# Performance work log

Measured on AMD Instinct MI355X. Metric: run time of the kernel, lower is better.

The kernel has to match this reference:

```python
import jax, jax.numpy as jnp
import numpy as np

S, B, H, T = 1024, 32, 1024, 512


def setup_inputs() -> dict:
    key = jax.random.key(0)
    ks = jax.random.split(key, 7)
    scale = 1.0 / np.sqrt(H)
    return {
        "hidden": jax.random.normal(ks[0], (S, B, H), dtype=jnp.float32),
        "x": jax.random.normal(ks[1], (B, T, H), dtype=jnp.float32),
        "problem_q": jax.random.normal(ks[2], (B, H), dtype=jnp.float32),
        "K_w": jax.random.normal(ks[3], (H, H), dtype=jnp.float32) * scale,
        "K_b": jax.random.normal(ks[4], (H,), dtype=jnp.float32) * scale,
        "V_w": jax.random.normal(ks[5], (H, H), dtype=jnp.float32) * scale,
        "V_b": jax.random.normal(ks[6], (H,), dtype=jnp.float32) * scale,
    }


def reference(hidden, x, problem_q, K_w, K_b, V_w, V_b):
    # hidden: [S, B, H] -> hidden2: [B, S, H]
    hidden2 = jnp.transpose(hidden, (1, 0, 2))
    # Linear projections (torch Linear: y = x @ W.T + b)
    k = jnp.einsum("bsh,kh->bsk", hidden2, K_w) + K_b  # [B, S, H]
    v = jnp.einsum("bsh,kh->bsk", hidden2, V_w) + V_b  # [B, S, H]
    # scores[b,t,s] = x[b,t] . k[b,s]  (QK^T per batch)
    scores = jnp.einsum("bth,bsh->bts", x, k)
    attn = jax.nn.softmax(scores, axis=-1)  # softmax over encoder positions S
    out = jax.nn.sigmoid(jnp.einsum("bts,bsh->bth", attn, v))  # [B, T, H]
    return out
```

## Files before the change

kernel.cpp:

```cpp
#include <hip/hip_runtime.h>

typedef unsigned short u16;
typedef __attribute__((ext_vector_type(8))) short short8;
typedef __attribute__((ext_vector_type(8))) _Float16 half8;
typedef __attribute__((ext_vector_type(4))) float f32x4;
typedef __attribute__((ext_vector_type(4))) u16 u16x4;
typedef __attribute__((ext_vector_type(4))) unsigned int u32x4;

#define DEVINL static __device__ __forceinline__

DEVINL u16 f2bf(float f) {
  unsigned u = __builtin_bit_cast(unsigned, f);
  u += 0x7fffu + ((u >> 16) & 1u);
  return (u16)(u >> 16);
}
DEVINL float bf2f(u16 h) {
  return __builtin_bit_cast(float, ((unsigned)h) << 16);
}
DEVINL u16 f2h(float f) { return __builtin_bit_cast(u16, (_Float16)f); }
DEVINL float h2f(u16 h) { return (float)__builtin_bit_cast(_Float16, h); }

DEVINL void gload16(const void* g, void* l) {
  __builtin_amdgcn_global_load_lds(
      (const __attribute__((address_space(1))) void*)g,
      (__attribute__((address_space(3))) void*)l, 16, 0, 0);
}

#define BAR() asm volatile("s_barrier" ::: "memory")
#define WAIT_VMN(n) asm volatile("s_waitcnt vmcnt(" #n ")" ::: "memory")
#define WAIT_VM_LGKM0() asm volatile("s_waitcnt vmcnt(0) lgkmcnt(0)" ::: "memory")


__global__ __launch_bounds__(512) void cvt_hidden2_k(const float* __restrict__ hid,
                                                     u16* __restrict__ hf,
                                                     u16* __restrict__ hT) {
  __shared__ u16 tl[64][136];
  const int s0 = blockIdx.x * 64;
  const int h0 = blockIdx.y * 128;
  const int b = blockIdx.z;
  const int t = threadIdx.x;
  const int r = t >> 5;
  const int c4 = (t & 31) * 4;
#pragma unroll
  for (int it = 0; it < 4; ++it) {
    const int s = it * 16 + r;
    const f32x4 v = *(const f32x4*)(hid + ((size_t)(s0 + s) * 32 + b) * 1024 + h0 + c4);
    u16x4 of;
    const int cs = c4 ^ (it << 2);
#pragma unroll
    for (int j = 0; j < 4; ++j) {
      of[j] = f2h(v[j]);
      tl[s][cs + j] = f2bf(v[j]);
    }
    *(u16x4*)(hf + ((size_t)b * 1024 + s0 + s) * 1024 + h0 + c4) = of;
  }
  __syncthreads();
  const int h = t >> 2;
  const int sq = (t & 3) * 16;
  u16 tmp[16] __attribute__((aligned(16)));
#pragma unroll
  for (int i = 0; i < 16; ++i)
    tmp[i] = tl[sq + i][h ^ ((((sq + i) >> 4) & 3) << 2)];
  u16* dst = hT + ((size_t)b * 1024 + h0 + h) * 1024 + s0 + sq;
  *(u32x4*)(dst) = *(const u32x4*)&tmp[0];
  *(u32x4*)(dst + 8) = *(const u32x4*)&tmp[8];
}

__global__ __launch_bounds__(256) void cvt_f32_bf16_k(const float* __restrict__ in,
                                                      u16* __restrict__ out, long n4) {
  long i = (long)blockIdx.x * 256 + threadIdx.x;
  const long stride = (long)gridDim.x * 256;
  for (; i < n4; i += stride) {
    const f32x4 v = ((const f32x4*)in)[i];
    u16x4 o;
#pragma unroll
    for (int j = 0; j < 4; ++j) o[j] = f2bf(v[j]);
    ((u16x4*)out)[i] = o;
  }
}

__global__ __launch_bounds__(256) void cvt_w_t_h_k(const float* __restrict__ in,
                                                   u16* __restrict__ out) {
  __shared__ float tile[64][65];
  const int bh = blockIdx.x * 64;
  const int bj = blockIdx.y * 64;
  const int t = threadIdx.x;
  const int r = t >> 4;
  const int c4 = (t & 15) * 4;
#pragma unroll
  for (int it = 0; it < 4; ++it) {
    const int row = it * 16 + r;
    const f32x4 v = *(const f32x4*)(in + (size_t)(bj + row) * 1024 + bh + c4);
#pragma unroll
    for (int j = 0; j < 4; ++j) tile[c4 + j][row] = v[j];
  }
  __syncthreads();
#pragma unroll
  for (int it = 0; it < 4; ++it) {
    const int hrow = it * 16 + r;
    u16x4 of;
#pragma unroll
    for (int j = 0; j < 4; ++j) of[j] = f2h(tile[hrow][c4 + j]);
    *(u16x4*)(out + (size_t)(bh + hrow) * 1024 + bj + c4) = of;
  }
}

__global__ __launch_bounds__(512) void gemm_qp_k(
    const float* __restrict__ X, const u16* __restrict__ Bm,
    u16* __restrict__ Chi, u16* __restrict__ Clo) {
  __shared__ u16 lA[2][256 * 64];
  __shared__ u16 lB[2][256 * 32];
  const int bid = blockIdx.x;
  const int swz = (bid & 7) * 32 + (bid >> 3);
  const int m0 = (swz >> 2) * 256;
  const int n0 = (swz & 3) * 256;
  const int tid = threadIdx.x;
  const int lane = tid & 63, wid = tid >> 6;
  const int wr = wid >> 2, wc = wid & 3;
  const int fr = lane & 15, fk = lane >> 4;

  f32x4 acc[8][4] = {};

#define STAGEAF(pb, kt)                                                        \
  {                                                                            \
    _Pragma("unroll") for (int j = 0; j < 2; ++j) {                            \
      const int ps = j * 512 + tid;                                            \
      const int r = ps >> 2, q = ps & 3;                                       \
      const float* src = X + (size_t)(m0 + r) * 1024 + (kt) * 32 + q * 8;      \
      const f32x4 v0 = *(const f32x4*)src;                                     \
      const f32x4 v1 = *(const f32x4*)(src + 4);                               \
      short8 hs, ls;                                                           \
      _Pragma("unroll") for (int e = 0; e < 4; ++e) {                          \
        const u16 a0 = f2h(v0[e]);                                             \
        const u16 a1 = f2h(v1[e]);                                             \
        hs[e] = (short)a0;                                                     \
        hs[e + 4] = (short)a1;                                                 \
        ls[e] = (short)f2h(v0[e] - h2f(a0));                                   \
        ls[e + 4] = (short)f2h(v1[e] - h2f(a1));                               \
      }                                                                        \
      const int c = q ^ (r & 7);                                               \
      *(short8*)&lA[pb][r * 64 + c * 8] = hs;                                  \
      *(short8*)&lA[pb][r * 64 + (c ^ 4) * 8] = ls;                            \
    }                                                                          \
  }
#define STAGEB(pb, kt)                                                         \
  {                                                                            \
    _Pragma("unroll") for (int j = 0; j < 2; ++j) {                            \
      const int slot = j * 512 + tid;                                          \
      const int r = slot >> 2;                                                 \
      const int g = (slot & 3) ^ ((r >> 1) & 3);                               \
      gload16(Bm + (size_t)(n0 + r) * 1024 + (kt) * 32 + g * 8,                \
              &lB[pb][(j * 512 + wid * 64) * 8]);                              \
    }                                                                          \
  }

  STAGEAF(0, 0);
  STAGEB(0, 0);

  for (int t = 0; t < 32; ++t) {
    const int p = t & 1;
    WAIT_VM_LGKM0();
    BAR();
    half8 bf[4];
#pragma unroll
    for (int nf = 0; nf < 4; ++nf) {
      const int rn = wc * 64 + nf * 16 + fr;
      const int cn = fk ^ ((rn >> 1) & 3);
      bf[nf] = *(const half8*)&lB[p][rn * 32 + cn * 8];
    }
    if (t < 31) {
      STAGEB(p ^ 1, t + 1);
      STAGEAF(p ^ 1, t + 1);
    }
#pragma unroll
    for (int ph = 0; ph < 4; ++ph) {
      half8 ah[2], al[2];
#pragma unroll
      for (int i = 0; i < 2; ++i) {
        const int r = wr * 128 + (ph * 2 + i) * 16 + fr;
        const int ch = fk ^ (r & 7);
        ah[i] = *(const half8*)&lA[p][r * 64 + ch * 8];
        al[i] = *(const half8*)&lA[p][r * 64 + (ch ^ 4) * 8];
      }
      __builtin_amdgcn_s_setprio(1);
#pragma unroll
      for (int i = 0; i < 2; ++i)
#pragma unroll
        for (int nf = 0; nf < 4; ++nf) {
          acc[ph * 2 + i][nf] =
              __builtin_amdgcn_mfma_f32_16x16x32_f16(ah[i], bf[nf], acc[ph * 2 + i][nf], 0, 0, 0);
          acc[ph * 2 + i][nf] =
              __builtin_amdgcn_mfma_f32_16x16x32_f16(al[i], bf[nf], acc[ph * 2 + i][nf], 0, 0, 0);
        }
      __builtin_amdgcn_s_setprio(0);
    }
  }
#undef STAGEAF
#undef STAGEB

  const int cb = n0 + wc * 64 + fr;
  const int rb = m0 + wr * 128 + fk * 4;
#pragma unroll
  for (int mf = 0; mf < 8; ++mf)
#pragma unroll
    for (int nf = 0; nf < 4; ++nf) {
      const int col = cb + nf * 16;
#pragma unroll
      for (int j = 0; j < 4; ++j) {
        const int row = rb + mf * 16 + j;
        const float kv = acc[mf][nf][j];
        const u16 hi = f2h(kv);
        Chi[(size_t)row * 1024 + col] = hi;
        Clo[(size_t)row * 1024 + col] = f2h(kv - h2f(hi));
      }
    }
}

__global__ __launch_bounds__(512) void gemm_sc_k(
    const u16* __restrict__ Qh_, const u16* __restrict__ Ql_,
    const u16* __restrict__ Hf_, float* __restrict__ S) {
  __shared__ u16 lA[3][256 * 64];
  __shared__ u16 lB[3][256 * 32];
  const int bid = blockIdx.x;
  const int swz = (bid & 7) * 32 + (bid >> 3);
  const int z = swz >> 3;
  const int m0 = ((swz >> 2) & 1) * 256;
  const int n0 = (swz & 3) * 256;
  const u16* Ah = Qh_ + (size_t)z * 512 * 1024;
  const u16* Al = Ql_ + (size_t)z * 512 * 1024;
  const u16* Bm = Hf_ + (size_t)z * 1024 * 1024;
  float* Cf = S + (size_t)z * 512 * 1024;
  const int tid = threadIdx.x;
  const int lane = tid & 63, wid = tid >> 6;
  const int wr = wid >> 2, wc = wid & 3;
  const int fr = lane & 15, fk = lane >> 4;

  f32x4 acc[8][4] = {};

#define STAGEA(pb, kt)                                                         \
  {                                                                            \
    _Pragma("unroll") for (int j = 0; j < 4; ++j) {                            \
      const int slot = j * 512 + tid;                                          \
      const int r = slot >> 3;                                                 \
      const int g = (slot & 7) ^ (r & 7);                                      \
      const u16* src = (g < 4) ? Ah : Al;                                      \
      gload16(src + (size_t)(m0 + r) * 1024 + (kt) * 32 + (g & 3) * 8,         \
              &lA[pb][(j * 512 + wid * 64) * 8]);                              \
    }                                                                          \
  }
#define STAGEB(pb, kt)                                                         \
  {                                                                            \
    _Pragma("unroll") for (int j = 0; j < 2; ++j) {                            \
      const int slot = j * 512 + tid;                                          \
      const int r = slot >> 2;                                                 \
      const int g = (slot & 3) ^ ((r >> 1) & 3);                               \
      gload16(Bm + (size_t)(n0 + r) * 1024 + (kt) * 32 + g * 8,                \
              &lB[pb][(j * 512 + wid * 64) * 8]);                              \
    }                                                                          \
  }

  STAGEA(0, 0);
  STAGEB(0, 0);
  STAGEA(1, 1);
  STAGEB(1, 1);

  int cur = 0;
  for (int t = 0; t < 32; ++t) {
    if (t < 31) {
      WAIT_VMN(6);
    } else {
      WAIT_VMN(0);
    }
    BAR();
    int pre = cur + 2;
    if (pre >= 3) pre -= 3;
    half8 bf[4];
#pragma unroll
    for (int nf = 0; nf < 4; ++nf) {
      const int rn = wc * 64 + nf * 16 + fr;
      const int cn = fk ^ ((rn >> 1) & 3);
      bf[nf] = *(const half8*)&lB[cur][rn * 32 + cn * 8];
    }
    if (t < 30) {
      STAGEA(pre, t + 2);
      STAGEB(pre, t + 2);
    }
#pragma unroll
    for (int ph = 0; ph < 4; ++ph) {
      half8 ah[2], al[2];
#pragma unroll
      for (int i = 0; i < 2; ++i) {
        const int r = wr * 128 + (ph * 2 + i) * 16 + fr;
        const int ch = fk ^ (r & 7);
        ah[i] = *(const half8*)&lA[cur][r * 64 + ch * 8];
        al[i] = *(const half8*)&lA[cur][r * 64 + (ch ^ 4) * 8];
      }
      __builtin_amdgcn_s_setprio(1);
#pragma unroll
      for (int i = 0; i < 2; ++i)
#pragma unroll
        for (int nf = 0; nf < 4; ++nf) {
          acc[ph * 2 + i][nf] =
              __builtin_amdgcn_mfma_f32_16x16x32_f16(ah[i], bf[nf], acc[ph * 2 + i][nf], 0, 0, 0);
          acc[ph * 2 + i][nf] =
              __builtin_amdgcn_mfma_f32_16x16x32_f16(al[i], bf[nf], acc[ph * 2 + i][nf], 0, 0, 0);
        }
      __builtin_amdgcn_s_setprio(0);
    }
    ++cur;
    if (cur == 3) cur = 0;
  }
#undef STAGEA
#undef STAGEB

  const int cb = n0 + wc * 64 + fr;
  const int rb = m0 + wr * 128 + fk * 4;
#pragma unroll
  for (int mf = 0; mf < 8; ++mf)
#pragma unroll
    for (int nf = 0; nf < 4; ++nf) {
      const int col = cb + nf * 16;
#pragma unroll
      for (int j = 0; j < 4; ++j) {
        const int row = rb + mf * 16 + j;
        Cf[(size_t)row * 1024 + col] = acc[mf][nf][j];
      }
    }
}

template <int CM>
__global__ __launch_bounds__(512) void gemm1_8ph_k(
    const u16* __restrict__ A_, const u16* __restrict__ Bt_,
    const float* __restrict__ bias, void* __restrict__ Cout) {
  __shared__ u16 lds[2][2][256 * 64];
  const int bid = blockIdx.x;
  const int swz = (bid & 7) * 32 + (bid >> 3);
  int m0, n0;
  const u16 *A, *Bt;
  float* Cf = nullptr;
  u16* Cb = nullptr;
  if (CM == 0) {
    const int z = swz >> 3;
    m0 = ((swz >> 2) & 1) * 256;
    n0 = (swz & 3) * 256;
    A = A_ + (size_t)z * 512 * 1024;
    Bt = Bt_ + (size_t)z * 1024 * 1024;
    Cb = (u16*)Cout + (size_t)z * 512 * 1024;
  } else {
    m0 = (swz >> 2) * 256;
    n0 = (swz & 3) * 256;
    A = A_; Bt = Bt_;
    Cf = (float*)Cout;
  }
  const int tid = threadIdx.x;
  const int lane = tid & 63, wid = tid >> 6;
  const int wr = wid >> 2, wc = wid & 3;
  const int fr = lane & 15, fk = lane >> 4;

  f32x4 acc[8][4] = {};

#define STAGE1(pb, q, gp, rb, kt)                                              \
  {                                                                            \
    _Pragma("unroll") for (int j = 0; j < 4; ++j) {                            \
      const int slot = j * 512 + tid;                                          \
      const int r = slot >> 3;                                                 \
      const int g = (slot & 7) ^ (r & 7);                                      \
      gload16((gp) + (size_t)((rb) + r) * 1024 + (kt) * 64 + g * 8,            \
              &lds[pb][q][(j * 512 + wid * 64) * 8]);                          \
    }                                                                          \
  }

  STAGE1(0, 0, A, m0, 0);
  STAGE1(0, 1, Bt, n0, 0);

  for (int t = 0; t < 16; ++t) {
    const int p = t & 1;
    WAIT_VMN(0);
    BAR();
    short8 bfr[4][2];
#pragma unroll
    for (int nf = 0; nf < 4; ++nf) {
      const int rn = wc * 64 + nf * 16 + fr;
#pragma unroll
      for (int ks = 0; ks < 2; ++ks) {
        const int g = (ks * 4 + fk) ^ (rn & 7);
        bfr[nf][ks] = *(const short8*)&lds[p][1][rn * 64 + g * 8];
      }
    }
    if (t < 15) {
      STAGE1(p ^ 1, 0, A, m0, t + 1);
      STAGE1(p ^ 1, 1, Bt, n0, t + 1);
    }
#pragma unroll
    for (int ph = 0; ph < 4; ++ph) {
      short8 a[2][2];
#pragma unroll
      for (int i = 0; i < 2; ++i) {
        const int r = wr * 128 + (ph * 2 + i) * 16 + fr;
#pragma unroll
        for (int ks = 0; ks < 2; ++ks) {
          const int g = (ks * 4 + fk) ^ (r & 7);
          a[i][ks] = *(const short8*)&lds[p][0][r * 64 + g * 8];
        }
      }
      __builtin_amdgcn_s_setprio(1);
#pragma unroll
      for (int i = 0; i < 2; ++i)
#pragma unroll
        for (int nf = 0; nf < 4; ++nf) {
          acc[ph * 2 + i][nf] = __builtin_amdgcn_mfma_f32_16x16x32_bf16(
              a[i][0], bfr[nf][0], acc[ph * 2 + i][nf], 0, 0, 0);
          acc[ph * 2 + i][nf] = __builtin_amdgcn_mfma_f32_16x16x32_bf16(
              a[i][1], bfr[nf][1], acc[ph * 2 + i][nf], 0, 0, 0);
        }
      __builtin_amdgcn_s_setprio(0);
    }
  }
#undef STAGE1

  const int cb = n0 + wc * 64 + fr;
  const int rb = m0 + wr * 128 + fk * 4;
  if (CM == 0) {
#pragma unroll
    for (int mf = 0; mf < 8; ++mf)
#pragma unroll
      for (int nf = 0; nf < 4; ++nf) {
        const int col = cb + nf * 16;
#pragma unroll
        for (int j = 0; j < 4; ++j) {
          const int row = rb + mf * 16 + j;
          Cb[(size_t)row * 1024 + col] = f2bf(acc[mf][nf][j]);
        }
      }
  } else {
#pragma unroll
    for (int mf = 0; mf < 8; ++mf)
#pragma unroll
      for (int nf = 0; nf < 4; ++nf) {
        const int col = cb + nf * 16;
        const float bv = bias[col];
#pragma unroll
        for (int j = 0; j < 4; ++j) {
          const int row = rb + mf * 16 + j;
          const float xv = acc[mf][nf][j] + bv;
          Cf[(size_t)row * 1024 + col] = 1.0f / (1.0f + __expf(-xv));
        }
      }
  }
}

__global__ __launch_bounds__(256) void softmax_k(const float* __restrict__ S,
                                                 u16* __restrict__ Attn) {
  const float* rp = S + (size_t)blockIdx.x * 1024;
  const int tid = threadIdx.x;
  const int lane = tid & 63, wid = tid >> 6;
  const f32x4 v = ((const f32x4*)rp)[tid];
  float mx = fmaxf(fmaxf(v[0], v[1]), fmaxf(v[2], v[3]));
#pragma unroll
  for (int off = 32; off; off >>= 1) mx = fmaxf(mx, __shfl_xor(mx, off));
  __shared__ float red[4];
  __shared__ float red2[4];
  if (lane == 0) red[wid] = mx;
  __syncthreads();
  mx = fmaxf(fmaxf(red[0], red[1]), fmaxf(red[2], red[3]));
  const float e0 = __expf(v[0] - mx), e1 = __expf(v[1] - mx);
  const float e2 = __expf(v[2] - mx), e3 = __expf(v[3] - mx);
  float s = (e0 + e1) + (e2 + e3);
#pragma unroll
  for (int off = 32; off; off >>= 1) s += __shfl_xor(s, off);
  if (lane == 0) red2[wid] = s;
  __syncthreads();
  const float inv = 1.0f / (red2[0] + red2[1] + red2[2] + red2[3]);
  u16x4 o;
  o[0] = f2bf(e0 * inv); o[1] = f2bf(e1 * inv); o[2] = f2bf(e2 * inv); o[3] = f2bf(e3 * inv);
  ((u16x4*)(Attn + (size_t)blockIdx.x * 1024))[tid] = o;
}

extern "C" void kernel_launch(void* const* d_in, const int* in_sizes, int n_in,
                              void* d_out, int out_size, void* d_ws, size_t ws_size,
                              hipStream_t stream) {
  const float* hidden = (const float*)d_in[0];
  const float* x = (const float*)d_in[1];
  const float* K_w = (const float*)d_in[3];
  const float* V_w = (const float*)d_in[5];
  const float* V_b = (const float*)d_in[6];

  char* ws = (char*)d_ws;
  u16* hf16 = (u16*)(ws);
  u16* hT = (u16*)(ws + 67108864);
  u16* qhi = (u16*)(ws + 134217728);
  u16* qlo = (u16*)(ws + 167772160);
  float* scoresF = (float*)(ws + 201326592);
  u16* attn = hf16;
  u16* ctx = qhi;
  u16* kwT = (u16*)(ws + 268435456);
  u16* vw = kwT + 1024 * 1024;
  float* out = (float*)d_out;

  cvt_hidden2_k<<<dim3(16, 8, 32), 512, 0, stream>>>(hidden, hf16, hT);
  cvt_w_t_h_k<<<dim3(16, 16), 256, 0, stream>>>(K_w, kwT);
  cvt_f32_bf16_k<<<1024, 256, 0, stream>>>(V_w, vw, 1024L * 1024 / 4);
  gemm_qp_k<<<256, 512, 0, stream>>>(x, kwT, qhi, qlo);
  gemm_sc_k<<<256, 512, 0, stream>>>(qhi, qlo, hf16, scoresF);
  softmax_k<<<16384, 256, 0, stream>>>(scoresF, attn);
  gemm1_8ph_k<0><<<256, 512, 0, stream>>>(attn, hT, nullptr, ctx);
  gemm1_8ph_k<1><<<256, 512, 0, stream>>>(ctx, vw, V_b, out);
}
```

Baseline: 321.5 us.

## Fuse hidden conversion, V_w conversion and Q projection GEMM into one heterogeneous kernel

Merges the hidden-state fp16/bf16 conversion, the V_w bf16 conversion and the query projection GEMM into a single launch. Blocks are split by block index into GEMM, transpose-conversion and weight-conversion roles. The memory-bound conversions then overlap with the compute-bound projection, and two launches go away. The GEMM tile shrinks from 256x256 to 256x128 so that 512 GEMM blocks are interleaved with the conversion blocks. That adds more redundant A-operand staging and a larger shared-memory footprint for every block, including the conversion-only ones.

```diff
diff --git a/kernel.cpp b/kernel.cpp
--- a/kernel.cpp
+++ b/kernel.cpp
@@ -30,54 +30,6 @@
 #define WAIT_VMN(n) asm volatile("s_waitcnt vmcnt(" #n ")" ::: "memory")
 #define WAIT_VM_LGKM0() asm volatile("s_waitcnt vmcnt(0) lgkmcnt(0)" ::: "memory")
 
-
-__global__ __launch_bounds__(512) void cvt_hidden2_k(const float* __restrict__ hid,
-                                                     u16* __restrict__ hf,
-                                                     u16* __restrict__ hT) {
-  __shared__ u16 tl[64][136];
-  const int s0 = blockIdx.x * 64;
-  const int h0 = blockIdx.y * 128;
-  const int b = blockIdx.z;
-  const int t = threadIdx.x;
-  const int r = t >> 5;
-  const int c4 = (t & 31) * 4;
-#pragma unroll
-  for (int it = 0; it < 4; ++it) {
-    const int s = it * 16 + r;
-    const f32x4 v = *(const f32x4*)(hid + ((size_t)(s0 + s) * 32 + b) * 1024 + h0 + c4);
-    u16x4 of;
-    const int cs = c4 ^ (it << 2);
-#pragma unroll
-    for (int j = 0; j < 4; ++j) {
-      of[j] = f2h(v[j]);
-      tl[s][cs + j] = f2bf(v[j]);
-    }
-    *(u16x4*)(hf + ((size_t)b * 1024 + s0 + s) * 1024 + h0 + c4) = of;
-  }
-  __syncthreads();
-  const int h = t >> 2;
-  const int sq = (t & 3) * 16;
-  u16 tmp[16] __attribute__((aligned(16)));
-#pragma unroll
-  for (int i = 0; i < 16; ++i)
-    tmp[i] = tl[sq + i][h ^ ((((sq + i) >> 4) & 3) << 2)];
-  u16* dst = hT + ((size_t)b * 1024 + h0 + h) * 1024 + s0 + sq;
-  *(u32x4*)(dst) = *(const u32x4*)&tmp[0];
-  *(u32x4*)(dst + 8) = *(const u32x4*)&tmp[8];
-}
-
-__global__ __launch_bounds__(256) void cvt_f32_bf16_k(const float* __restrict__ in,
-                                                      u16* __restrict__ out, long n4) {
-  long i = (long)blockIdx.x * 256 + threadIdx.x;
-  const long stride = (long)gridDim.x * 256;
-  for (; i < n4; i += stride) {
-    const f32x4 v = ((const f32x4*)in)[i];
-    u16x4 o;
-#pragma unroll
-    for (int j = 0; j < 4; ++j) o[j] = f2bf(v[j]);
-    ((u16x4*)out)[i] = o;
-  }
-}
 
 __global__ __launch_bounds__(256) void cvt_w_t_h_k(const float* __restrict__ in,
                                                    u16* __restrict__ out) {
@@ -105,21 +57,25 @@
   }
 }
 
-__global__ __launch_bounds__(512) void gemm_qp_k(
-    const float* __restrict__ X, const u16* __restrict__ Bm,
+__global__ __launch_bounds__(512) void front_k(
+    const float* __restrict__ hid, const float* __restrict__ X,
+    const u16* __restrict__ kwT, const float* __restrict__ Vw,
+    u16* __restrict__ hf, u16* __restrict__ hT, u16* __restrict__ vw,
     u16* __restrict__ Chi, u16* __restrict__ Clo) {
-  __shared__ u16 lA[2][256 * 64];
-  __shared__ u16 lB[2][256 * 32];
+  __shared__ u16 smem[40960];
   const int bid = blockIdx.x;
-  const int swz = (bid & 7) * 32 + (bid >> 3);
-  const int m0 = (swz >> 2) * 256;
-  const int n0 = (swz & 3) * 256;
   const int tid = threadIdx.x;
-  const int lane = tid & 63, wid = tid >> 6;
-  const int wr = wid >> 2, wc = wid & 3;
-  const int fr = lane & 15, fk = lane >> 4;
-
-  f32x4 acc[8][4] = {};
+
+  if (bid < 1024 && (bid & 1) == 0) {
+    const int qid = bid >> 1;
+    const int swz = (qid & 7) * 64 + (qid >> 3);
+    const int m0 = (swz >> 3) * 256;
+    const int n0 = (swz & 7) * 128;
+    const int lane = tid & 63, wid = tid >> 6;
+    const int wr = wid >> 2, wc = wid & 3;
+    const int fr = lane & 15, fk = lane >> 4;
+
+    f32x4 acc[8][2] = {};
 
 #define STAGEAF(pb, kt)                                                        \
   {                                                                            \
@@ -139,81 +95,120 @@
         ls[e + 4] = (short)f2h(v1[e] - h2f(a1));                               \
       }                                                                        \
       const int c = q ^ (r & 7);                                               \
-      *(short8*)&lA[pb][r * 64 + c * 8] = hs;                                  \
-      *(short8*)&lA[pb][r * 64 + (c ^ 4) * 8] = ls;                            \
+      *(short8*)&smem[(pb) * 16384 + r * 64 + c * 8] = hs;                     \
+      *(short8*)&smem[(pb) * 16384 + r * 64 + (c ^ 4) * 8] = ls;               \
     }                                                                          \
   }
 #define STAGEB(pb, kt)                                                         \
   {                                                                            \
-    _Pragma("unroll") for (int j = 0; j < 2; ++j) {                            \
-      const int slot = j * 512 + tid;                                          \
-      const int r = slot >> 2;                                                 \
-      const int g = (slot & 3) ^ ((r >> 1) & 3);                               \
-      gload16(Bm + (size_t)(n0 + r) * 1024 + (kt) * 32 + g * 8,                \
-              &lB[pb][(j * 512 + wid * 64) * 8]);                              \
-    }                                                                          \
-  }
-
-  STAGEAF(0, 0);
-  STAGEB(0, 0);
-
-  for (int t = 0; t < 32; ++t) {
-    const int p = t & 1;
-    WAIT_VM_LGKM0();
-    BAR();
-    half8 bf[4];
-#pragma unroll
-    for (int nf = 0; nf < 4; ++nf) {
-      const int rn = wc * 64 + nf * 16 + fr;
-      const int cn = fk ^ ((rn >> 1) & 3);
-      bf[nf] = *(const half8*)&lB[p][rn * 32 + cn * 8];
-    }
-    if (t < 31) {
-      STAGEB(p ^ 1, t + 1);
-      STAGEAF(p ^ 1, t + 1);
-    }
-#pragma unroll
-    for (int ph = 0; ph < 4; ++ph) {
-      half8 ah[2], al[2];
-#pragma unroll
-      for (int i = 0; i < 2; ++i) {
-        const int r = wr * 128 + (ph * 2 + i) * 16 + fr;
-        const int ch = fk ^ (r & 7);
-        ah[i] = *(const half8*)&lA[p][r * 64 + ch * 8];
-        al[i] = *(const half8*)&lA[p][r * 64 + (ch ^ 4) * 8];
-      }
-      __builtin_amdgcn_s_setprio(1);
-#pragma unroll
-      for (int i = 0; i < 2; ++i)
-#pragma unroll
-        for (int nf = 0; nf < 4; ++nf) {
-          acc[ph * 2 + i][nf] =
-              __builtin_amdgcn_mfma_f32_16x16x32_f16(ah[i], bf[nf], acc[ph * 2 + i][nf], 0, 0, 0);
-          acc[ph * 2 + i][nf] =
-              __builtin_amdgcn_mfma_f32_16x16x32_f16(al[i], bf[nf], acc[ph * 2 + i][nf], 0, 0, 0);
-        }
-      __builtin_amdgcn_s_setprio(0);
-    }
-  }
+    const int slot = tid;                                                      \
+    const int r = slot >> 2;                                                   \
+    const int g = (slot & 3) ^ ((r >> 1) & 3);                                 \
+    gload16(kwT + (size_t)(n0 + r) * 1024 + (kt) * 32 + g * 8,                 \
+            &smem[32768 + (pb) * 4096 + (wid * 64) * 8]);                      \
+  }
+
+    STAGEAF(0, 0);
+    STAGEB(0, 0);
+
+    for (int t = 0; t < 32; ++t) {
+      const int p = t & 1;
+      WAIT_VM_LGKM0();
+      BAR();
+      half8 bf[2];
+#pragma unroll
+      for (int nf = 0; nf < 2; ++nf) {
+        const int rn = wc * 32 + nf * 16 + fr;
+        const int cn = fk ^ ((rn >> 1) & 3);
+        bf[nf] = *(const half8*)&smem[32768 + p * 4096 + rn * 32 + cn * 8];
+      }
+      if (t < 31) {
+        STAGEB(p ^ 1, t + 1);
+        STAGEAF(p ^ 1, t + 1);
+      }
+#pragma unroll
+      for (int ph = 0; ph < 4; ++ph) {
+        half8 ah[2], al[2];
+#pragma unroll
+        for (int i = 0; i < 2; ++i) {
+          const int r = wr * 128 + (ph * 2 + i) * 16 + fr;
+          const int ch = fk ^ (r & 7);
+          ah[i] = *(const half8*)&smem[p * 16384 + r * 64 + ch * 8];
+          al[i] = *(const half8*)&smem[p * 16384 + r * 64 + (ch ^ 4) * 8];
+        }
+        __builtin_amdgcn_s_setprio(1);
+#pragma unroll
+        for (int i = 0; i < 2; ++i)
+#pragma unroll
+          for (int nf = 0; nf < 2; ++nf) {
+            acc[ph * 2 + i][nf] = __builtin_amdgcn_mfma_f32_16x16x32_f16(
+                ah[i], bf[nf], acc[ph * 2 + i][nf], 0, 0, 0);
+            acc[ph * 2 + i][nf] = __builtin_amdgcn_mfma_f32_16x16x32_f16(
+                al[i], bf[nf], acc[ph * 2 + i][nf], 0, 0, 0);
+          }
+        __builtin_amdgcn_s_setprio(0);
+      }
+    }
 #undef STAGEAF
 #undef STAGEB
 
-  const int cb = n0 + wc * 64 + fr;
-  const int rb = m0 + wr * 128 + fk * 4;
-#pragma unroll
-  for (int mf = 0; mf < 8; ++mf)
-#pragma unroll
-    for (int nf = 0; nf < 4; ++nf) {
-      const int col = cb + nf * 16;
+    const int cb = n0 + wc * 32 + fr;
+    const int rb = m0 + wr * 128 + fk * 4;
+#pragma unroll
+    for (int mf = 0; mf < 8; ++mf)
+#pragma unroll
+      for (int nf = 0; nf < 2; ++nf) {
+        const int col = cb + nf * 16;
+#pragma unroll
+        for (int j = 0; j < 4; ++j) {
+          const int row = rb + mf * 16 + j;
+          const float kv = acc[mf][nf][j];
+          const u16 hi = f2h(kv);
+          Chi[(size_t)row * 1024 + col] = hi;
+          Clo[(size_t)row * 1024 + col] = f2h(kv - h2f(hi));
+        }
+      }
+  } else if (bid < 4608) {
+    const int cid = (bid < 1024) ? (bid >> 1) : (512 + (bid - 1024));
+    const int s0 = (cid & 15) * 64;
+    const int h0 = ((cid >> 4) & 7) * 128;
+    const int b = cid >> 7;
+    u16(*tl)[136] = (u16(*)[136])smem;
+    const int r = tid >> 5;
+    const int c4 = (tid & 31) * 4;
+#pragma unroll
+    for (int it = 0; it < 4; ++it) {
+      const int s = it * 16 + r;
+      const f32x4 v = *(const f32x4*)(hid + ((size_t)(s0 + s) * 32 + b) * 1024 + h0 + c4);
+      u16x4 of;
+      const int cs = c4 ^ (it << 2);
 #pragma unroll
       for (int j = 0; j < 4; ++j) {
-        const int row = rb + mf * 16 + j;
-        const float kv = acc[mf][nf][j];
-        const u16 hi = f2h(kv);
-        Chi[(size_t)row * 1024 + col] = hi;
-        Clo[(size_t)row * 1024 + col] = f2h(kv - h2f(hi));
-      }
-    }
+        of[j] = f2h(v[j]);
+        tl[s][cs + j] = f2bf(v[j]);
+      }
+      *(u16x4*)(hf + ((size_t)b * 1024 + s0 + s) * 1024 + h0 + c4) = of;
+    }
+    __syncthreads();
+    const int h = tid >> 2;
+    const int sq = (tid & 3) * 16;
+    u16 tmp[16] __attribute__((aligned(16)));
+#pragma unroll
+    for (int i = 0; i < 16; ++i)
+      tmp[i] = tl[sq + i][h ^ ((((sq + i) >> 4) & 3) << 2)];
+    u16* dst = hT + ((size_t)b * 1024 + h0 + h) * 1024 + s0 + sq;
+    *(u32x4*)(dst) = *(const u32x4*)&tmp[0];
+    *(u32x4*)(dst + 8) = *(const u32x4*)&tmp[8];
+  } else {
+    long i = (long)(bid - 4608) * 512 + tid;
+    for (; i < 262144; i += 131072) {
+      const f32x4 v = ((const f32x4*)Vw)[i];
+      u16x4 o;
+#pragma unroll
+      for (int j = 0; j < 4; ++j) o[j] = f2bf(v[j]);
+      ((u16x4*)vw)[i] = o;
+    }
+  }
 }
 
 __global__ __launch_bounds__(512) void gemm_sc_k(
@@ -497,10 +492,8 @@
   u16* vw = kwT + 1024 * 1024;
   float* out = (float*)d_out;
 
-  cvt_hidden2_k<<<dim3(16, 8, 32), 512, 0, stream>>>(hidden, hf16, hT);
   cvt_w_t_h_k<<<dim3(16, 16), 256, 0, stream>>>(K_w, kwT);
-  cvt_f32_bf16_k<<<1024, 256, 0, stream>>>(V_w, vw, 1024L * 1024 / 4);
-  gemm_qp_k<<<256, 512, 0, stream>>>(x, kwT, qhi, qlo);
+  front_k<<<4864, 512, 0, stream>>>(hidden, x, kwT, V_w, hf16, hT, vw, qhi, qlo);
   gemm_sc_k<<<256, 512, 0, stream>>>(qhi, qlo, hf16, scoresF);
   softmax_k<<<16384, 256, 0, stream>>>(scoresF, attn);
   gemm1_8ph_k<0><<<256, 512, 0, stream>>>(attn, hT, nullptr, ctx);
```

Result: slower. 394.0 us (+22.6%).

## Retile scores GEMM to 128x256 tiles with BK=64 double buffering and 512 blocks

Applied to the files above, without the earlier changes.

The scores GEMM (split-fp16 Q times hidden) changes from 256x256 output tiles with a 3-stage BK=32 pipeline to 128x256 tiles with a 2-stage BK=64 pipeline, launching 512 blocks instead of 256. More blocks spread across the CUs and fewer accumulators per thread should lift occupancy and shorten the tail, and the deeper K step halves the number of barriers. In exchange, reuse per block drops because B tiles are loaded twice as often. Each iteration also waits for all outstanding loads (vmcnt 0), which may expose load latency compared with the old 3-deep prefetch.

```diff
diff --git a/kernel.cpp b/kernel.cpp
--- a/kernel.cpp
+++ b/kernel.cpp
@@ -219,12 +219,12 @@
 __global__ __launch_bounds__(512) void gemm_sc_k(
     const u16* __restrict__ Qh_, const u16* __restrict__ Ql_,
     const u16* __restrict__ Hf_, float* __restrict__ S) {
-  __shared__ u16 lA[3][256 * 64];
-  __shared__ u16 lB[3][256 * 32];
+  __shared__ u16 lA[2][128 * 128];
+  __shared__ u16 lB[2][256 * 64];
   const int bid = blockIdx.x;
-  const int swz = (bid & 7) * 32 + (bid >> 3);
-  const int z = swz >> 3;
-  const int m0 = ((swz >> 2) & 1) * 256;
+  const int swz = (bid & 7) * 64 + (bid >> 3);
+  const int z = swz >> 4;
+  const int m0 = ((swz >> 2) & 3) * 128;
   const int n0 = (swz & 3) * 256;
   const u16* Ah = Qh_ + (size_t)z * 512 * 1024;
   const u16* Al = Ql_ + (size_t)z * 512 * 1024;
@@ -235,88 +235,82 @@
   const int wr = wid >> 2, wc = wid & 3;
   const int fr = lane & 15, fk = lane >> 4;
 
-  f32x4 acc[8][4] = {};
+  f32x4 acc[4][4] = {};
 
 #define STAGEA(pb, kt)                                                         \
+  {                                                                            \
+    _Pragma("unroll") for (int j = 0; j < 4; ++j) {                            \
+      const int slot = j * 512 + tid;                                          \
+      const int r = slot >> 4;                                                 \
+      const int g = (slot & 15) ^ (r & 7);                                     \
+      const u16* src = (g < 8) ? Ah : Al;                                      \
+      gload16(src + (size_t)(m0 + r) * 1024 + (kt) * 64 + (g & 7) * 8,         \
+              &lA[pb][slot * 8]);                                              \
+    }                                                                          \
+  }
+#define STAGEB(pb, kt)                                                         \
   {                                                                            \
     _Pragma("unroll") for (int j = 0; j < 4; ++j) {                            \
       const int slot = j * 512 + tid;                                          \
       const int r = slot >> 3;                                                 \
       const int g = (slot & 7) ^ (r & 7);                                      \
-      const u16* src = (g < 4) ? Ah : Al;                                      \
-      gload16(src + (size_t)(m0 + r) * 1024 + (kt) * 32 + (g & 3) * 8,         \
-              &lA[pb][(j * 512 + wid * 64) * 8]);                              \
-    }                                                                          \
-  }
-#define STAGEB(pb, kt)                                                         \
-  {                                                                            \
-    _Pragma("unroll") for (int j = 0; j < 2; ++j) {                            \
-      const int slot = j * 512 + tid;                                          \
-      const int r = slot >> 2;                                                 \
-      const int g = (slot & 3) ^ ((r >> 1) & 3);                               \
-      gload16(Bm + (size_t)(n0 + r) * 1024 + (kt) * 32 + g * 8,                \
-              &lB[pb][(j * 512 + wid * 64) * 8]);                              \
+      gload16(Bm + (size_t)(n0 + r) * 1024 + (kt) * 64 + g * 8,                \
+              &lB[pb][slot * 8]);                                              \
     }                                                                          \
   }
 
   STAGEA(0, 0);
   STAGEB(0, 0);
-  STAGEA(1, 1);
-  STAGEB(1, 1);
-
-  int cur = 0;
-  for (int t = 0; t < 32; ++t) {
-    if (t < 31) {
-      WAIT_VMN(6);
-    } else {
-      WAIT_VMN(0);
-    }
+
+  for (int t = 0; t < 16; ++t) {
+    const int p = t & 1;
+    WAIT_VMN(0);
     BAR();
-    int pre = cur + 2;
-    if (pre >= 3) pre -= 3;
-    half8 bf[4];
+    half8 bf[4][2];
 #pragma unroll
     for (int nf = 0; nf < 4; ++nf) {
       const int rn = wc * 64 + nf * 16 + fr;
-      const int cn = fk ^ ((rn >> 1) & 3);
-      bf[nf] = *(const half8*)&lB[cur][rn * 32 + cn * 8];
-    }
-    if (t < 30) {
-      STAGEA(pre, t + 2);
-      STAGEB(pre, t + 2);
-    }
-#pragma unroll
-    for (int ph = 0; ph < 4; ++ph) {
+#pragma unroll
+      for (int ks = 0; ks < 2; ++ks) {
+        const int c = (ks * 4 + fk) ^ (rn & 7);
+        bf[nf][ks] = *(const half8*)&lB[p][rn * 64 + c * 8];
+      }
+    }
+    if (t < 15) {
+      STAGEA(p ^ 1, t + 1);
+      STAGEB(p ^ 1, t + 1);
+    }
+#pragma unroll
+    for (int mf = 0; mf < 4; ++mf) {
+      const int r = wr * 64 + mf * 16 + fr;
       half8 ah[2], al[2];
 #pragma unroll
-      for (int i = 0; i < 2; ++i) {
-        const int r = wr * 128 + (ph * 2 + i) * 16 + fr;
-        const int ch = fk ^ (r & 7);
-        ah[i] = *(const half8*)&lA[cur][r * 64 + ch * 8];
-        al[i] = *(const half8*)&lA[cur][r * 64 + (ch ^ 4) * 8];
+      for (int ks = 0; ks < 2; ++ks) {
+        const int kc = ks * 4 + fk;
+        const int ch = kc ^ (r & 7);
+        ah[ks] = *(const half8*)&lA[p][r * 128 + ch * 8];
+        al[ks] = *(const half8*)&lA[p][r * 128 + (ch + 8) * 8];
       }
       __builtin_amdgcn_s_setprio(1);
 #pragma unroll
-      for (int i = 0; i < 2; ++i)
-#pragma unroll
-        for (int nf = 0; nf < 4; ++nf) {
-          acc[ph * 2 + i][nf] =
-              __builtin_amdgcn_mfma_f32_16x16x32_f16(ah[i], bf[nf], acc[ph * 2 + i][nf], 0, 0, 0);
-          acc[ph * 2 + i][nf] =
-              __builtin_amdgcn_mfma_f32_16x16x32_f16(al[i], bf[nf], acc[ph * 2 + i][nf], 0, 0, 0);
+      for (int nf = 0; nf < 4; ++nf)
+#pragma unroll
+        for (int ks = 0; ks < 2; ++ks) {
+          acc[mf][nf] = __builtin_amdgcn_mfma_f32_16x16x32_f16(
+              ah[ks], bf[nf][ks], acc[mf][nf], 0, 0, 0);
+          acc[mf][nf] = __builtin_amdgcn_mfma_f32_16x16x32_f16(
+              al[ks], bf[nf][ks], acc[mf][nf], 0, 0, 0);
         }
       __builtin_amdgcn_s_setprio(0);
     }
-    ++cur;
-    if (cur == 3) cur = 0;
   }
 #undef STAGEA
 #undef STAGEB
 
   const int cb = n0 + wc * 64 + fr;
-  const int rb = m0 + wr * 128 + fk * 4;
-#pragma unroll
-  for (int mf = 0; mf < 8; ++mf)
+  const int rb = m0 + wr * 64 + fk * 4;
+#pragma unroll
+  for (int mf = 0; mf < 4; ++mf)
 #pragma unroll
     for (int nf = 0; nf < 4; ++nf) {
       const int col = cb + nf * 16;
@@ -501,7 +495,7 @@
   cvt_w_t_h_k<<<dim3(16, 16), 256, 0, stream>>>(K_w, kwT);
   cvt_f32_bf16_k<<<1024, 256, 0, stream>>>(V_w, vw, 1024L * 1024 / 4);
   gemm_qp_k<<<256, 512, 0, stream>>>(x, kwT, qhi, qlo);
-  gemm_sc_k<<<256, 512, 0, stream>>>(qhi, qlo, hf16, scoresF);
+  gemm_sc_k<<<512, 512, 0, stream>>>(qhi, qlo, hf16, scoresF);
   softmax_k<<<16384, 256, 0, stream>>>(scoresF, attn);
   gemm1_8ph_k<0><<<256, 512, 0, stream>>>(attn, hT, nullptr, ctx);
   gemm1_8ph_k<1><<<256, 512, 0, stream>>>(ctx, vw, V_b, out);
```

After: 335.1 us. 4.2% more time.
